# Kernel tuning notes

Measured on AMD Instinct MI355X. Metric: run time of the kernel, lower is better.

The kernel has to match this reference:

```python
import jax, jax.numpy as jnp
import numpy as np

STRIDES = (8, 16, 32, 64, 128)
SCORE_THRESH = 0.05
IOU_THRESH = 0.6
MAX_DET = 1000


def _flat(p):
    # [B,C,H,W] -> [B,H*W,C]
    B, C = p.shape[0], p.shape[1]
    return jnp.transpose(p, (0, 2, 3, 1)).reshape(B, -1, C)


def _coords(h, w, stride):
    # FCOS coords_fmap2orig: center of each stride cell, (x, y) order -> [h*w, 2]
    sx = (jnp.arange(w, dtype=jnp.float32) * stride + stride // 2)
    sy = (jnp.arange(h, dtype=jnp.float32) * stride + stride // 2)
    yy, xx = jnp.meshgrid(sy, sx, indexing='ij')
    return jnp.stack([xx.ravel(), yy.ravel()], axis=-1)


def _nms_keep(boxes, valid, thr):
    # boxes: [M,4] sorted by descending score; valid: [M] bool. Greedy NMS keep mask.
    x1, y1, x2, y2 = boxes[:, 0], boxes[:, 1], boxes[:, 2], boxes[:, 3]
    area = (x2 - x1 + 1.0) * (y2 - y1 + 1.0)
    xx1 = jnp.maximum(x1[:, None], x1[None, :])
    yy1 = jnp.maximum(y1[:, None], y1[None, :])
    xx2 = jnp.minimum(x2[:, None], x2[None, :])
    yy2 = jnp.minimum(y2[:, None], y2[None, :])
    inter = jnp.clip(xx2 - xx1, 0.0) * jnp.clip(yy2 - yy1, 0.0)
    iou = inter / (area[:, None] + area[None, :] - inter)
    M = boxes.shape[0]
    idx = jnp.arange(M)

    def body(i, keep):
        sup = (idx > i) & (iou[i] > thr) & keep[i]
        return keep & (~sup)

    return jax.lax.fori_loop(0, M, body, valid)


def setup_inputs() -> dict:
    key = jax.random.key(0)
    B, C = 16, 80
    sizes = [(128, 128), (64, 64), (32, 32), (16, 16), (8, 8)]
    ks = jax.random.split(key, 15)
    inp = {}
    for i, (h, w) in enumerate(sizes):
        lvl = i + 3
        inp[f'cls_p{lvl}'] = jax.random.normal(ks[3 * i], (B, C, h, w), jnp.float32)
        inp[f'cnt_p{lvl}'] = jax.random.normal(ks[3 * i + 1], (B, 1, h, w), jnp.float32)
        inp[f'reg_p{lvl}'] = jax.random.uniform(ks[3 * i + 2], (B, 4, h, w), jnp.float32) * 100.0
    return inp


def _detect(cls_levels, cnt_levels, reg_levels):
    cls_logits = jnp.concatenate([_flat(p) for p in cls_levels], axis=1)  # [B,N,80]
    cnt_logits = jnp.concatenate([_flat(p) for p in cnt_levels], axis=1)  # [B,N,1]
    reg_preds = jnp.concatenate([_flat(p) for p in reg_levels], axis=1)   # [B,N,4]
    coords = jnp.concatenate(
        [_coords(p.shape[2], p.shape[3], s) for p, s in zip(cls_levels, STRIDES)], axis=0)  # [N,2]

    cls_preds = jax.nn.sigmoid(cls_logits)
    cnt_preds = jax.nn.sigmoid(cnt_logits)[..., 0]                        # [B,N]
    cls_max = jnp.max(cls_preds, axis=-1)                                 # [B,N]
    cls_classes = jnp.argmax(cls_preds, axis=-1) + 1                      # [B,N] 1-based labels
    scores = jnp.sqrt(cls_max * cnt_preds)                                # add_centerness

    boxes = jnp.concatenate(
        [coords[None] - reg_preds[..., :2], coords[None] + reg_preds[..., 2:]], axis=-1)  # [B,N,4]

    M = min(MAX_DET, scores.shape[1])
    topv, topi = jax.lax.top_k(scores, M)                                 # sorted desc
    classes_k = jnp.take_along_axis(cls_classes, topi, axis=1)            # [B,M]
    boxes_k = jnp.take_along_axis(boxes, topi[..., None], axis=1)         # [B,M,4]
    valid = topv >= SCORE_THRESH

    def per_image(b, s, c, v):
        # class-aware NMS via coordinate offset trick
        off = c.astype(b.dtype) * (jnp.max(b) + 1.0)
        keep = _nms_keep(b + off[:, None], v, IOU_THRESH)
        kf = keep.astype(s.dtype)
        return s * kf, c * keep.astype(c.dtype), b * kf[:, None]

    return jax.vmap(per_image)(boxes_k, topv, classes_k, valid)


def reference(cls_p3, cnt_p3, reg_p3, cls_p4, cnt_p4, reg_p4, cls_p5, cnt_p5, reg_p5,
              cls_p6, cnt_p6, reg_p6, cls_p7, cnt_p7, reg_p7):
    cls_levels = [cls_p3, cls_p4, cls_p5, cls_p6, cls_p7]
    cnt_levels = [cnt_p3, cnt_p4, cnt_p5, cnt_p6, cnt_p7]
    reg_levels = [reg_p3, reg_p4, reg_p5, reg_p6, reg_p7]
    return _detect(cls_levels, cnt_levels, reg_levels)
```

## Files before the change

kernel.cpp:

```cpp
#include <hip/hip_runtime.h>
#include <hip/hip_bf16.h>
#include <math.h>

#define NB 16
#define NC 80
#define NA 21824
#define NM 1000
#define NHBINS 16384
#define CANDCAP 4096

#define OFF_KEYS     0ul
#define OFF_CLSV     2793472ul
#define OFF_HIST     4190208ul
#define OFF_CANDCNT  5238784ul
#define OFF_MAXB     5238848ul
#define OFF_CANDS    5238912ul
#define OFF_TOPSCORE 5763200ul
#define OFF_TOPCLS   5827200ul
#define OFF_TOPBOX   5891200ul
#define OFF_MASK     6147200ul

__device__ __forceinline__ float sigm(float x) { return 1.0f / (1.0f + expf(-x)); }

__global__ __launch_bounds__(256, 4) void k_score(
    const float* __restrict__ cls3, const float* __restrict__ cnt3,
    const float* __restrict__ cls4, const float* __restrict__ cnt4,
    const float* __restrict__ cls5, const float* __restrict__ cnt5,
    const float* __restrict__ cls6, const float* __restrict__ cnt6,
    const float* __restrict__ cls7, const float* __restrict__ cnt7,
    unsigned long long* __restrict__ keys,
    float* __restrict__ clsv, unsigned int* __restrict__ hist)
{
    __shared__ unsigned int histpk[NHBINS / 2];
    __shared__ float lm[4 * 64 * 4];
    __shared__ int   lam[4 * 64 * 4];
    __shared__ float cm[256];
    __shared__ int   cam[256];
    const int b = blockIdx.y;
    const int tid = threadIdx.x;
    const int a = tid & 63, s = tid >> 6;
    const int g4 = blockIdx.x * 64 + a;

    for (int i = tid; i < NHBINS / 2; i += 256) histpk[i] = 0u;

    if (g4 < (NA >> 2)) {
        const int n = g4 << 2;
        const float* clsP; int off, logW;
        if      (n < 16384) { clsP = cls3; off = 0;     logW = 7; }
        else if (n < 20480) { clsP = cls4; off = 16384; logW = 6; }
        else if (n < 21504) { clsP = cls5; off = 20480; logW = 5; }
        else if (n < 21760) { clsP = cls6; off = 21504; logW = 4; }
        else                { clsP = cls7; off = 21760; logW = 3; }
        const int HW4 = 1 << (2 * logW - 2);
        const int l4 = (n - off) >> 2;
        const float4* cp = (const float4*)clsP + (size_t)b * NC * HW4 + l4;
        const int c0 = s * 20;
        float4 v[20];
#pragma unroll
        for (int u = 0; u < 20; u++) v[u] = cp[(size_t)(c0 + u) * HW4];
        float m[4] = { v[0].x, v[0].y, v[0].z, v[0].w };
        int am[4] = { c0, c0, c0, c0 };
#pragma unroll
        for (int u = 1; u < 20; u++) {
            const int c = c0 + u;
            if (v[u].x > m[0]) { m[0] = v[u].x; am[0] = c; }
            if (v[u].y > m[1]) { m[1] = v[u].y; am[1] = c; }
            if (v[u].z > m[2]) { m[2] = v[u].z; am[2] = c; }
            if (v[u].w > m[3]) { m[3] = v[u].w; am[3] = c; }
        }
#pragma unroll
        for (int k = 0; k < 4; k++) { lm[tid * 4 + k] = m[k]; lam[tid * 4 + k] = am[k]; }
    }
    __syncthreads();
    if (tid < 64 && (blockIdx.x * 64 + tid) < (NA >> 2)) {
        float M[4]; int AM[4];
#pragma unroll
        for (int k = 0; k < 4; k++) { M[k] = lm[tid * 4 + k]; AM[k] = lam[tid * 4 + k]; }
        for (int s2 = 1; s2 < 4; s2++) {
#pragma unroll
            for (int k = 0; k < 4; k++) {
                float vv = lm[(s2 * 64 + tid) * 4 + k];
                if (vv > M[k]) { M[k] = vv; AM[k] = lam[(s2 * 64 + tid) * 4 + k]; }
            }
        }
#pragma unroll
        for (int k = 0; k < 4; k++) { cm[tid * 4 + k] = M[k]; cam[tid * 4 + k] = AM[k]; }
    }
    __syncthreads();
    const int n2 = blockIdx.x * 256 + tid;
    if (n2 < NA) {
        const float* cntP; int off, logW;
        if      (n2 < 16384) { cntP = cnt3; off = 0;     logW = 7; }
        else if (n2 < 20480) { cntP = cnt4; off = 16384; logW = 6; }
        else if (n2 < 21504) { cntP = cnt5; off = 20480; logW = 5; }
        else if (n2 < 21760) { cntP = cnt6; off = 21504; logW = 4; }
        else                 { cntP = cnt7; off = 21760; logW = 3; }
        const int HW = 1 << (2 * logW);
        const int local = n2 - off;
        float cn = cntP[(size_t)b * HW + local];
        float M = cm[tid]; int AM = cam[tid];
        float sc = sqrtf(sigm(M) * sigm(cn));
        unsigned long long key = ((unsigned long long)__float_as_uint(sc) << 32)
                               | (unsigned int)(~(unsigned int)n2);
        keys[(size_t)b * NA + n2] = key;
        unsigned int bin = (unsigned int)(key >> 50);
        atomicAdd(&histpk[bin >> 1], (bin & 1u) ? 0x10000u : 1u);
        clsv[(size_t)b * NA + n2] = (float)(AM + 1);
    }
    __syncthreads();
    unsigned int* gh = hist + b * NHBINS;
    for (int i = tid; i < NHBINS / 2; i += 256) {
        unsigned int pk = histpk[i];
        if (pk) {
            unsigned int lo = pk & 0xFFFFu, hi = pk >> 16;
            if (lo) atomicAdd(&gh[2 * i], lo);
            if (hi) atomicAdd(&gh[2 * i + 1], hi);
        }
    }
}

__global__ __launch_bounds__(256) void k_compact(
    const unsigned long long* __restrict__ keys, const unsigned int* __restrict__ hist,
    unsigned int* __restrict__ candcnt, unsigned long long* __restrict__ cands)
{
    __shared__ int part1[256];
    __shared__ int part2[8];
    __shared__ int sBoundary;
    __shared__ unsigned int lcount;
    __shared__ unsigned int lbase;
    const int b = blockIdx.y;
    const int tid = threadIdx.x;
    const unsigned int* h = hist + b * NHBINS;
    int sum = 0;
    for (int i = 0; i < 64; i++) sum += (int)h[tid * 64 + i];
    part1[tid] = sum;
    if (tid == 0) lcount = 0u;
    __syncthreads();
    if (tid < 8) { int s2 = 0; for (int t = 0; t < 32; t++) s2 += part1[tid * 32 + t]; part2[tid] = s2; }
    __syncthreads();
    if (tid == 0) {
        int acc = 0, sc;
        for (sc = 7; sc > 0; sc--) { if (acc + part2[sc] >= NM) break; acc += part2[sc]; }
        int t;
        for (t = sc * 32 + 31; t > sc * 32; t--) { if (acc + part1[t] >= NM) break; acc += part1[t]; }
        int bin;
        for (bin = t * 64 + 63; bin > t * 64; bin--) { if (acc + (int)h[bin] >= NM) break; acc += (int)h[bin]; }
        sBoundary = bin;
    }
    __syncthreads();
    const unsigned int boundary = (unsigned int)sBoundary;
    unsigned long long hk[4]; unsigned int hslot[4]; int nh = 0;
    for (int nn = blockIdx.x * 256 + tid; nn < NA; nn += 22 * 256) {
        unsigned long long key = keys[(size_t)b * NA + nn];
        if ((unsigned int)(key >> 50) >= boundary) {
            hslot[nh] = atomicAdd(&lcount, 1u);
            hk[nh] = key;
            nh++;
        }
    }
    __syncthreads();
    if (tid == 0) lbase = atomicAdd(&candcnt[b], lcount);
    __syncthreads();
    const unsigned int base = lbase;
    for (int t = 0; t < nh; t++) {
        unsigned int pos = base + hslot[t];
        if (pos < CANDCAP) cands[(size_t)b * CANDCAP + pos] = hk[t];
    }
}

__global__ __launch_bounds__(256) void k_rank(
    const unsigned long long* __restrict__ cands, const unsigned int* __restrict__ candcnt,
    const float* __restrict__ clsv,
    const float* __restrict__ reg3, const float* __restrict__ reg4, const float* __restrict__ reg5,
    const float* __restrict__ reg6, const float* __restrict__ reg7,
    float* __restrict__ topscore, float* __restrict__ topcls,
    float4* __restrict__ topbox, unsigned int* __restrict__ maxbEnc)
{
    __shared__ unsigned long long sbuf[CANDCAP];
    __shared__ unsigned int redmax[256];
    const int b = blockIdx.y;
    int cnt = (int)candcnt[b]; if (cnt > CANDCAP) cnt = CANDCAP;
    const int base = blockIdx.x * 256;
    if (base >= cnt) return;
    const int tid = threadIdx.x;
    for (int i = tid; i < cnt; i += 256) sbuf[i] = cands[(size_t)b * CANDCAP + i];
    __syncthreads();
    const int idx = base + tid;
    unsigned int enc = 0;
    if (idx < cnt) {
        const unsigned long long key = sbuf[idx];
        const unsigned int ai = ~(unsigned int)key;
        const float* regP; int off, W, logW, st;
        if      (ai < 16384) { regP = reg3; off = 0;     W = 128; logW = 7; st = 8;   }
        else if (ai < 20480) { regP = reg4; off = 16384; W = 64;  logW = 6; st = 16;  }
        else if (ai < 21504) { regP = reg5; off = 20480; W = 32;  logW = 5; st = 32;  }
        else if (ai < 21760) { regP = reg6; off = 21504; W = 16;  logW = 4; st = 64;  }
        else                 { regP = reg7; off = 21760; W = 8;   logW = 3; st = 128; }
        const int local = (int)ai - off;
        const int HW = 1 << (2 * logW);
        const float* rp = regP + (size_t)b * 4 * HW + local;
        float r0 = rp[0], r1 = rp[HW], r2 = rp[2 * HW], r3 = rp[3 * HW];
        float cv = clsv[(size_t)b * NA + ai];
        int rank = 0;
        int j = 0;
        for (; j + 4 <= cnt; j += 4) {
            rank += (sbuf[j] > key) + (sbuf[j+1] > key) + (sbuf[j+2] > key) + (sbuf[j+3] > key);
        }
        for (; j < cnt; j++) rank += (sbuf[j] > key);
        if (rank < NM) {
            const float hs = (float)(st >> 1);
            float cx = (float)((local & (W - 1)) * st) + hs;
            float cy = (float)((local >> logW) * st) + hs;
            float4 bx = make_float4(cx - r0, cy - r1, cx + r2, cy + r3);
            topscore[b * NM + rank] = __uint_as_float((unsigned int)(key >> 32));
            topcls[b * NM + rank] = cv;
            topbox[b * NM + rank] = bx;
            float mx = fmaxf(fmaxf(bx.x, bx.y), fmaxf(bx.z, bx.w));
            unsigned int ub = __float_as_uint(mx);
            enc = (ub & 0x80000000u) ? ~ub : (ub | 0x80000000u);
        }
    }
    redmax[tid] = enc;
    __syncthreads();
    for (int sgap = 128; sgap > 0; sgap >>= 1) {
        if (tid < sgap) { unsigned int o = redmax[tid + sgap]; if (o > redmax[tid]) redmax[tid] = o; }
        __syncthreads();
    }
    if (tid == 0 && redmax[0]) atomicMax(&maxbEnc[b], redmax[0]);
}

__global__ __launch_bounds__(256) void k_iou(
    const float4* __restrict__ topbox, const float* __restrict__ topcls,
    const unsigned int* __restrict__ maxbEnc, unsigned long long* __restrict__ maskArr)
{
    __shared__ float4 sB[NM];
    __shared__ float sA[NM];
    const int b = blockIdx.y;
    const int tid = threadIdx.x;
    unsigned int enc = maxbEnc[b];
    unsigned int ub = (enc & 0x80000000u) ? (enc & 0x7FFFFFFFu) : ~enc;
    const float mp1 = __fadd_rn(__uint_as_float(ub), 1.0f);
    for (int r = tid; r < NM; r += 256) {
        float4 f = topbox[b * NM + r];
        float off = __fmul_rn(topcls[b * NM + r], mp1);
        f.x = __fadd_rn(f.x, off); f.y = __fadd_rn(f.y, off);
        f.z = __fadd_rn(f.z, off); f.w = __fadd_rn(f.w, off);
        sB[r] = f;
        sA[r] = __fmul_rn(__fadd_rn(__fsub_rn(f.z, f.x), 1.0f),
                          __fadd_rn(__fsub_rn(f.w, f.y), 1.0f));
    }
    __syncthreads();
    int task = blockIdx.x * 256 + tid;
    if (task >= NM * 16) return;
    int i = task >> 4, w = task & 15;
    float4 bi = sB[i]; float ai = sA[i];
    unsigned long long bits = 0ULL;
    int j0 = w << 6;
    int jstart = (j0 > i + 1) ? j0 : i + 1;
    int jend = (j0 + 64 < NM) ? j0 + 64 : NM;
    for (int j = jstart; j < jend; j++) {
        float4 bj = sB[j];
        float xx1 = fmaxf(bi.x, bj.x);
        float yy1 = fmaxf(bi.y, bj.y);
        float xx2 = fminf(bi.z, bj.z);
        float yy2 = fminf(bi.w, bj.w);
        float iw = fmaxf(__fsub_rn(xx2, xx1), 0.0f);
        float ih = fmaxf(__fsub_rn(yy2, yy1), 0.0f);
        float inter = __fmul_rn(iw, ih);
        float denom = __fsub_rn(__fadd_rn(ai, sA[j]), inter);
        float iou = inter / denom;
        if (iou > 0.6f) bits |= (1ULL << (j - j0));
    }
    maskArr[((size_t)b * NM + i) * 16 + w] = bits;
}

__global__ __launch_bounds__(256) void k_nms_sweep(
    const unsigned long long* __restrict__ maskArr,
    const float* __restrict__ topscore, const float* __restrict__ topcls,
    const float4* __restrict__ topbox, float* __restrict__ out)
{
    __shared__ unsigned long long sdiag[16][64];
    __shared__ unsigned long long lremv[16];
    __shared__ unsigned long long skeep;
    const int b = blockIdx.x;
    const int tid = threadIdx.x;
    const int j = tid & 63, q = tid >> 6;
    const unsigned long long* gmask = maskArr + (size_t)b * (NM * 16);

    if (tid < 16) lremv[tid] = 0ULL;
    for (int idx = tid; idx < 1024; idx += 256) {
        int w = idx >> 6, jj = idx & 63;
        int row = w * 64 + jj;
        sdiag[w][jj] = (row < NM) ? gmask[(size_t)row * 16 + w] : 0ULL;
    }
    __syncthreads();
    for (int r = tid; r < NM; r += 256) {
        float s = topscore[b * NM + r];
        if (!(s >= 0.05f)) atomicOr(&lremv[r >> 6], 1ULL << (r & 63));
    }
    __syncthreads();

    for (int w = 0; w < 16; w++) {
        unsigned long long vals[4]; int ks[4]; int nk = 0;
        const int row = w * 64 + j;
        for (int k = w + 1 + q; k < 16; k += 4) {
            ks[nk] = k;
            vals[nk] = (row < NM) ? gmask[(size_t)row * 16 + k] : 0ULL;
            nk++;
        }
        if (tid < 64) {
            unsigned long long D = sdiag[w][j];
            unsigned int dlo = (unsigned int)D, dhi = (unsigned int)(D >> 32);
            unsigned long long sv = lremv[w];
            unsigned int slo = __builtin_amdgcn_readfirstlane((unsigned int)sv);
            unsigned int shi = __builtin_amdgcn_readfirstlane((unsigned int)(sv >> 32));
            unsigned long long s = ((unsigned long long)shi << 32) | slo;
#pragma unroll
            for (int bb = 0; bb < 64; bb++) {
                unsigned int rlo = __builtin_amdgcn_readlane(dlo, bb);
                unsigned int rhi = __builtin_amdgcn_readlane(dhi, bb);
                unsigned long long rowv = ((unsigned long long)rhi << 32) | rlo;
                if (!((s >> bb) & 1ULL)) s |= rowv;
            }
            if (j == 0) { lremv[w] = s; skeep = ~s; }
        }
        __syncthreads();
        unsigned long long kw = skeep;
        for (int t2 = 0; t2 < nk; t2++) {
            unsigned long long v = ((kw >> j) & 1ULL) ? vals[t2] : 0ULL;
#pragma unroll
            for (int off2 = 32; off2 >= 1; off2 >>= 1) v |= __shfl_xor(v, off2, 64);
            if (j == 0) atomicOr(&lremv[ks[t2]], v);
        }
        __syncthreads();
    }

    for (int r = tid; r < NM; r += 256) {
        bool keep = !((lremv[r >> 6] >> (r & 63)) & 1ULL);
        float kf = keep ? 1.0f : 0.0f;
        out[b * NM + r] = topscore[b * NM + r] * kf;
        out[NB * NM + b * NM + r] = topcls[b * NM + r] * kf;
        float4 bx = topbox[b * NM + r];
        ((float4*)(out + 2 * NB * NM))[b * NM + r] = make_float4(bx.x * kf, bx.y * kf, bx.z * kf, bx.w * kf);
    }
}

extern "C" void kernel_launch(void* const* d_in, const int* in_sizes, int n_in,
                              void* d_out, int out_size, void* d_ws, size_t ws_size,
                              hipStream_t stream) {
    const float* cls3 = (const float*)d_in[0];
    const float* cnt3 = (const float*)d_in[1];
    const float* reg3 = (const float*)d_in[2];
    const float* cls4 = (const float*)d_in[3];
    const float* cnt4 = (const float*)d_in[4];
    const float* reg4 = (const float*)d_in[5];
    const float* cls5 = (const float*)d_in[6];
    const float* cnt5 = (const float*)d_in[7];
    const float* reg5 = (const float*)d_in[8];
    const float* cls6 = (const float*)d_in[9];
    const float* cnt6 = (const float*)d_in[10];
    const float* reg6 = (const float*)d_in[11];
    const float* cls7 = (const float*)d_in[12];
    const float* cnt7 = (const float*)d_in[13];
    const float* reg7 = (const float*)d_in[14];

    char* ws = (char*)d_ws;
    unsigned long long* keys   = (unsigned long long*)(ws + OFF_KEYS);
    float*              clsv   = (float*)(ws + OFF_CLSV);
    unsigned int*       hist   = (unsigned int*)(ws + OFF_HIST);
    unsigned int*       candcnt= (unsigned int*)(ws + OFF_CANDCNT);
    unsigned int*       maxbE  = (unsigned int*)(ws + OFF_MAXB);
    unsigned long long* cands  = (unsigned long long*)(ws + OFF_CANDS);
    float*              topsc  = (float*)(ws + OFF_TOPSCORE);
    float*              topcl  = (float*)(ws + OFF_TOPCLS);
    float4*             topbx  = (float4*)(ws + OFF_TOPBOX);
    unsigned long long* maskA  = (unsigned long long*)(ws + OFF_MASK);

    hipMemsetAsync(ws + OFF_HIST, 0, (size_t)(NB * NHBINS * 4 + 128), stream);

    dim3 g1(86, NB);
    k_score<<<g1, 256, 0, stream>>>(cls3, cnt3, cls4, cnt4, cls5, cnt5,
                                    cls6, cnt6, cls7, cnt7,
                                    keys, clsv, hist);
    dim3 g2(22, NB);
    k_compact<<<g2, 256, 0, stream>>>(keys, hist, candcnt, cands);
    dim3 g3(CANDCAP / 256, NB);
    k_rank<<<g3, 256, 0, stream>>>(cands, candcnt, clsv, reg3, reg4, reg5, reg6, reg7,
                                   topsc, topcl, topbx, maxbE);
    dim3 g4(63, NB);
    k_iou<<<g4, 256, 0, stream>>>(topbx, topcl, maxbE, maskA);
    k_nms_sweep<<<NB, 256, 0, stream>>>(maskA, topsc, topcl, topbx, (float*)d_out);
}
```

Baseline: 303.7 us.

## Transpose NMS mask to word-major layout and stage whole mask in LDS for sweep

The IoU mask kernel now writes its bitmask as [batch][word][row] instead of [batch][row][word], which makes the stores coalesced across consecutive rows. The sweep kernel copies the full 128KB per-image mask into shared memory with 16-byte vector loads. It then runs the diagonal resolve redundantly in all four waves, which drops one barrier per word and replaces the shuffle reduction with direct LDS atomicOr from kept rows. The large LDS allocation cuts occupancy to one block per CU and adds an upfront copy, but only 16 blocks run anyway.

Result: faster. 270.9 us (-10.8%).

```diff
diff --git a/kernel.cpp b/kernel.cpp
--- a/kernel.cpp
+++ b/kernel.cpp
@@ -252,7 +252,7 @@
     __syncthreads();
     int task = blockIdx.x * 256 + tid;
     if (task >= NM * 16) return;
-    int i = task >> 4, w = task & 15;
+    int w = task / NM, i = task - w * NM;
     float4 bi = sB[i]; float ai = sA[i];
     unsigned long long bits = 0ULL;
     int j0 = w << 6;
@@ -271,7 +271,7 @@
         float iou = inter / denom;
         if (iou > 0.6f) bits |= (1ULL << (j - j0));
     }
-    maskArr[((size_t)b * NM + i) * 16 + w] = bits;
+    maskArr[((size_t)b * 16 + w) * NM + i] = bits;
 }
 
 __global__ __launch_bounds__(256) void k_nms_sweep(
@@ -279,61 +279,52 @@
     const float* __restrict__ topscore, const float* __restrict__ topcls,
     const float4* __restrict__ topbox, float* __restrict__ out)
 {
-    __shared__ unsigned long long sdiag[16][64];
+    __shared__ unsigned long long smask[16 * NM];
     __shared__ unsigned long long lremv[16];
-    __shared__ unsigned long long skeep;
     const int b = blockIdx.x;
     const int tid = threadIdx.x;
     const int j = tid & 63, q = tid >> 6;
-    const unsigned long long* gmask = maskArr + (size_t)b * (NM * 16);
-
+    const unsigned long long* gmask = maskArr + (size_t)b * (16 * NM);
+
+    {
+        const ulonglong2* src = (const ulonglong2*)gmask;
+        ulonglong2* dst = (ulonglong2*)smask;
+        for (int idx = tid; idx < 8 * NM; idx += 256) dst[idx] = src[idx];
+    }
     if (tid < 16) lremv[tid] = 0ULL;
-    for (int idx = tid; idx < 1024; idx += 256) {
-        int w = idx >> 6, jj = idx & 63;
-        int row = w * 64 + jj;
-        sdiag[w][jj] = (row < NM) ? gmask[(size_t)row * 16 + w] : 0ULL;
-    }
     __syncthreads();
     for (int r = tid; r < NM; r += 256) {
         float s = topscore[b * NM + r];
         if (!(s >= 0.05f)) atomicOr(&lremv[r >> 6], 1ULL << (r & 63));
     }
-    __syncthreads();
 
     for (int w = 0; w < 16; w++) {
-        unsigned long long vals[4]; int ks[4]; int nk = 0;
+        __syncthreads();
         const int row = w * 64 + j;
-        for (int k = w + 1 + q; k < 16; k += 4) {
-            ks[nk] = k;
-            vals[nk] = (row < NM) ? gmask[(size_t)row * 16 + k] : 0ULL;
-            nk++;
-        }
-        if (tid < 64) {
-            unsigned long long D = sdiag[w][j];
-            unsigned int dlo = (unsigned int)D, dhi = (unsigned int)(D >> 32);
-            unsigned long long sv = lremv[w];
-            unsigned int slo = __builtin_amdgcn_readfirstlane((unsigned int)sv);
-            unsigned int shi = __builtin_amdgcn_readfirstlane((unsigned int)(sv >> 32));
-            unsigned long long s = ((unsigned long long)shi << 32) | slo;
-#pragma unroll
-            for (int bb = 0; bb < 64; bb++) {
-                unsigned int rlo = __builtin_amdgcn_readlane(dlo, bb);
-                unsigned int rhi = __builtin_amdgcn_readlane(dhi, bb);
-                unsigned long long rowv = ((unsigned long long)rhi << 32) | rlo;
-                if (!((s >> bb) & 1ULL)) s |= rowv;
+        unsigned long long D = (row < NM) ? smask[w * NM + row] : 0ULL;
+        unsigned int dlo = (unsigned int)D, dhi = (unsigned int)(D >> 32);
+        unsigned long long sv = lremv[w];
+        unsigned int slo = __builtin_amdgcn_readfirstlane((unsigned int)sv);
+        unsigned int shi = __builtin_amdgcn_readfirstlane((unsigned int)(sv >> 32));
+        unsigned long long s = ((unsigned long long)shi << 32) | slo;
+#pragma unroll
+        for (int bb = 0; bb < 64; bb++) {
+            unsigned int rlo = __builtin_amdgcn_readlane(dlo, bb);
+            unsigned int rhi = __builtin_amdgcn_readlane(dhi, bb);
+            unsigned long long rowv = ((unsigned long long)rhi << 32) | rlo;
+            unsigned long long t = s | rowv;
+            s = ((s >> bb) & 1ULL) ? s : t;
+        }
+        if (tid == 0) lremv[w] = s;
+        const unsigned long long kw = ~s;
+        if ((kw >> j) & 1ULL) {
+            for (int k = w + 1 + q; k < 16; k += 4) {
+                unsigned long long v = (row < NM) ? smask[k * NM + row] : 0ULL;
+                if (v) atomicOr(&lremv[k], v);
             }
-            if (j == 0) { lremv[w] = s; skeep = ~s; }
-        }
-        __syncthreads();
-        unsigned long long kw = skeep;
-        for (int t2 = 0; t2 < nk; t2++) {
-            unsigned long long v = ((kw >> j) & 1ULL) ? vals[t2] : 0ULL;
-#pragma unroll
-            for (int off2 = 32; off2 >= 1; off2 >>= 1) v |= __shfl_xor(v, off2, 64);
-            if (j == 0) atomicOr(&lremv[ks[t2]], v);
-        }
-        __syncthreads();
-    }
+        }
+    }
+    __syncthreads();
 
     for (int r = tid; r < NM; r += 256) {
         bool keep = !((lremv[r >> 6] >> (r & 63)) & 1ULL);
```
